# Optimization experiments

Hardware: AMD Instinct MI355X
Metric: run time of the kernel (lower is better)

The kernel has to match this reference:

```python
import jax, jax.numpy as jnp
import numpy as np

PC_RANGE = [-51.2, -51.2, -5.0, 51.2, 51.2, 3.0]
VOXEL = [0.1, 0.1, 0.2]
OSF = 8
NUM_PRIOR = 100
C = 256
BN_EPS = 1e-5
LN_EPS = 1e-5


def _conv(x, w, pad):
    # x: [B,C,H,W], w: [O,I,kh,kw]
    return jax.lax.conv_general_dilated(
        x, w, window_strides=(1, 1), padding=[(pad, pad), (pad, pad)],
        dimension_numbers=('NCHW', 'OIHW', 'NCHW'))


def _bn(x, g, b, m, v):
    scale = (g / jnp.sqrt(v + BN_EPS))[None, :, None, None]
    return (x - m[None, :, None, None]) * scale + b[None, :, None, None]


def setup_inputs() -> dict:
    key = jax.random.key(0)
    ks = jax.random.split(key, 24)
    s3 = 1.0 / np.sqrt(C * 9)
    s1 = 1.0 / np.sqrt(C)
    inp = {
        'bev_feat': jax.random.normal(ks[0], (4, C, 128, 128), jnp.float32),
        'template_anchor': jax.random.normal(ks[1], (4, 900, 11), jnp.float32),
        # shared_conv: 3x3 conv (no bias) + BN(eval) + ReLU
        'shared_w': jax.random.normal(ks[2], (C, C, 3, 3), jnp.float32) * s3,
        'bn1_g': jax.random.normal(ks[3], (C,), jnp.float32) * 0.1 + 1.0,
        'bn1_b': jax.random.normal(ks[4], (C,), jnp.float32) * 0.1,
        'bn1_m': jax.random.normal(ks[5], (C,), jnp.float32) * 0.1,
        'bn1_v': jax.random.uniform(ks[6], (C,), jnp.float32) + 0.5,
        # objectness: 3x3 conv (no bias) + BN + ReLU + 1x1 conv (bias=-2)
        'obj_w1': jax.random.normal(ks[7], (C, C, 3, 3), jnp.float32) * s3,
        'bn2_g': jax.random.normal(ks[8], (C,), jnp.float32) * 0.1 + 1.0,
        'bn2_b': jax.random.normal(ks[9], (C,), jnp.float32) * 0.1,
        'bn2_m': jax.random.normal(ks[10], (C,), jnp.float32) * 0.1,
        'bn2_v': jax.random.uniform(ks[11], (C,), jnp.float32) + 0.5,
        'obj_w2': jax.random.normal(ks[12], (1, C, 1, 1), jnp.float32) * s1,
        'obj_b2': jnp.full((1,), -2.0, jnp.float32),
        # feat_proj: Linear + LN + ReLU + Linear
        'fp_w1': jax.random.normal(ks[13], (C, C), jnp.float32) * s1,
        'fp_b1': jax.random.normal(ks[14], (C,), jnp.float32) * 0.01,
        'ln_g': jnp.ones((C,), jnp.float32),
        'ln_b': jnp.zeros((C,), jnp.float32),
        'fp_w2': jax.random.normal(ks[15], (C, C), jnp.float32) * s1,
        'fp_b2': jax.random.normal(ks[16], (C,), jnp.float32) * 0.01,
        # geometry heads (1x1 convs, bias init 0)
        'z_w': jax.random.normal(ks[17], (1, C, 1, 1), jnp.float32) * s1,
        'z_b': jnp.zeros((1,), jnp.float32),
        'dim_w': jax.random.normal(ks[18], (3, C, 1, 1), jnp.float32) * s1,
        'dim_b': jnp.zeros((3,), jnp.float32),
        'yaw_w': jax.random.normal(ks[19], (2, C, 1, 1), jnp.float32) * s1,
        'yaw_b': jnp.zeros((2,), jnp.float32),
        'vel_w': jax.random.normal(ks[20], (2, C, 1, 1), jnp.float32) * s1,
        'vel_b': jnp.zeros((2,), jnp.float32),
    }
    return inp


def _forward(bev_feat, template_anchor, shared_w, bn1_g, bn1_b, bn1_m, bn1_v,
             obj_w1, bn2_g, bn2_b, bn2_m, bn2_v, obj_w2, obj_b2,
             fp_w1, fp_b1, ln_g, ln_b, fp_w2, fp_b2,
             z_w, z_b, dim_w, dim_b, yaw_w, yaw_b, vel_w, vel_b):
    B, Cc, H, W = bev_feat.shape
    # shared_conv
    feat = jax.nn.relu(_bn(_conv(bev_feat, shared_w, 1), bn1_g, bn1_b, bn1_m, bn1_v))
    # objectness heatmap
    h = jax.nn.relu(_bn(_conv(feat, obj_w1, 1), bn2_g, bn2_b, bn2_m, bn2_v))
    heatmap = jax.nn.sigmoid(_conv(h, obj_w2, 0) + obj_b2[None, :, None, None])
    score = heatmap.reshape(B, H * W)
    K = min(NUM_PRIOR, H * W, template_anchor.shape[1])
    topk_score, topk_inds = jax.lax.top_k(score, K)  # [B,K]
    ys = topk_inds // W
    xs = topk_inds % W
    # gather BEV features at topk locations: [B,K,C]
    feat_flat = feat.reshape(B, Cc, H * W).transpose(0, 2, 1)
    gathered = jnp.take_along_axis(feat_flat, topk_inds[:, :, None], axis=1)
    # feat_proj: Linear + LN + ReLU + Linear
    x = gathered @ fp_w1.T + fp_b1
    mu = jnp.mean(x, axis=-1, keepdims=True)
    var = jnp.mean((x - mu) ** 2, axis=-1, keepdims=True)
    x = (x - mu) / jnp.sqrt(var + LN_EPS) * ln_g + ln_b
    x = jax.nn.relu(x)
    prior_feature = x @ fp_w2.T + fp_b2
    prior_feature = prior_feature * (1.0 + topk_score[:, :, None])
    # geometry heads (1x1 convs == linear on gathered features)
    z_pred = gathered @ z_w[:, :, 0, 0].T + z_b      # [B,K,1]
    dim_pred = gathered @ dim_w[:, :, 0, 0].T + dim_b  # [B,K,3]
    yaw_pred = gathered @ yaw_w[:, :, 0, 0].T + yaw_b  # [B,K,2]
    vel_pred = gathered @ vel_w[:, :, 0, 0].T + vel_b  # [B,K,2]
    # anchor update
    pa = template_anchor[:, :K, :]
    x_metric = (xs.astype(pa.dtype) + 0.5) * (VOXEL[0] * OSF) + PC_RANGE[0]
    y_metric = (ys.astype(pa.dtype) + 0.5) * (VOXEL[1] * OSF) + PC_RANGE[1]
    z_new = pa[..., 2] + 0.5 * z_pred[..., 0]
    dims_new = pa[..., 3:6] + 0.2 * jnp.clip(dim_pred, -1.0, 1.0)
    yaw = jnp.tanh(yaw_pred)
    nrm = jnp.maximum(jnp.sqrt(jnp.sum(yaw * yaw, axis=-1, keepdims=True)), 1e-6)
    yaw_new = 0.7 * pa[..., 6:8] + 0.3 * (yaw / nrm)
    vel_new = pa[..., 8:10] + 0.2 * jnp.clip(vel_pred, -2.0, 2.0)
    prior_anchor = jnp.concatenate([
        x_metric[..., None], y_metric[..., None], z_new[..., None],
        dims_new, yaw_new, vel_new, pa[..., 10:]], axis=-1)
    return prior_feature, prior_anchor, topk_score


def reference(bev_feat, template_anchor, shared_w, bn1_g, bn1_b, bn1_m, bn1_v,
              obj_w1, bn2_g, bn2_b, bn2_m, bn2_v, obj_w2, obj_b2,
              fp_w1, fp_b1, ln_g, ln_b, fp_w2, fp_b2,
              z_w, z_b, dim_w, dim_b, yaw_w, yaw_b, vel_w, vel_b):
    return _forward(bev_feat, template_anchor, shared_w, bn1_g, bn1_b, bn1_m, bn1_v,
                    obj_w1, bn2_g, bn2_b, bn2_m, bn2_v, obj_w2, obj_b2,
                    fp_w1, fp_b1, ln_g, ln_b, fp_w2, fp_b2,
                    z_w, z_b, dim_w, dim_b, yaw_w, yaw_b, vel_w, vel_b)
```

## Files before the change

kernel.cpp:

```cpp
#include <hip/hip_runtime.h>
#include <math.h>


typedef __attribute__((ext_vector_type(8))) short bf16x8;
typedef __attribute__((ext_vector_type(4))) float f32x4;

#define HW 16384
#define WPITCH 130
#define CCAP 192
#define PSTR 28
#define WSO_XN    0ULL
#define WSO_FEATB 34078720ULL
#define WSO_WP1   68157440ULL
#define WSO_WP2   69337088ULL
#define WSO_BNP   70516736ULL
#define WSO_LOG   70521856ULL
#define WSO_CAND  70784000ULL
#define WSO_CNT   70787072ULL
#define WSO_EXL   70787136ULL
#define WSO_TIDX  70790208ULL
#define WSO_TLOG  70791808ULL
#define WSO_W1N   70793408ULL
#define WSO_W2N   73152704ULL
#define WSO_A1P   WSO_XN
#define WSO_ACC2  28311552ULL

__device__ __forceinline__ float bf2f(short s) {
  return __uint_as_float(((unsigned)(unsigned short)s) << 16);
}
__device__ __forceinline__ short f2bf(float f) {
  unsigned u = __float_as_uint(f);
  u += 0x7fffu + ((u >> 16) & 1u);
  return (short)(u >> 16);
}
__device__ __forceinline__ void gll16(const void* g, void* l) {
  __builtin_amdgcn_global_load_lds(
      (const __attribute__((address_space(1))) void*)g,
      (__attribute__((address_space(3))) void*)l, 16, 0, 0);
}

__global__ void wprep2(const float* __restrict__ s1, const float* __restrict__ s2,
                       short* __restrict__ wp1, short* __restrict__ wp2,
                       float* __restrict__ wn1, float* __restrict__ wn2) {
  int bx = blockIdx.x;
  const float* src;
  short* wp;
  float* wn;
  if (bx >= 2304) {
    src = s2; wp = wp2; wn = wn2; bx -= 2304;
  } else {
    src = s1; wp = wp1; wn = wn1;
  }
  int i = bx * 256 + threadIdx.x;
  float v = src[i];
  int k = i % 9;
  int r = i / 9;
  int ci = r & 255;
  int co = r >> 8;
  wp[(k * 256 + co) * 256 + ci] = f2bf(v);
  wn[(ci * 9 + k) * 256 + co] = v;
}

__global__ void smallprep(const float* g1, const float* b1, const float* m1,
                          const float* v1, const float* g2, const float* b2,
                          const float* m2, const float* v2, const float* w2,
                          const float* ob2, float* __restrict__ bnp,
                          short* __restrict__ xn, short* __restrict__ featb,
                          float* __restrict__ logits) {
  const int blk = blockIdx.x, t = threadIdx.x;
  if (blk < 1024) {
    int i = blk * 256 + t;
    int c = i & 255;
    int r = i >> 8;
    int nh = r >> 1;
    int side = r & 1;
    size_t off = ((size_t)nh * WPITCH + (side ? 129 : 0)) * 256 + c;
    xn[off] = 0;
    featb[off] = 0;
  } else if (blk < 1280) {
    logits[(blk - 1024) * 256 + t] = ob2[0];
  } else {
    float s1 = g1[t] / sqrtf(v1[t] + 1e-5f);
    bnp[t] = s1;
    bnp[256 + t] = b1[t] - m1[t] * s1;
    float s2 = g2[t] / sqrtf(v2[t] + 1e-5f);
    bnp[512 + t] = s2;
    bnp[768 + t] = b2[t] - m2[t] * s2;
    bnp[1024 + t] = w2[t];
  }
}

__global__ __launch_bounds__(256) void nchw2nhwc(const float* __restrict__ in,
                                                 short* __restrict__ out) {
  __shared__ short tl[64 * 66];
  int n = blockIdx.z, c0 = blockIdx.y * 64, s0 = blockIdx.x * 64;
  int sl = threadIdx.x & 63, cl = threadIdx.x >> 6;
  for (int p = 0; p < 16; ++p) {
    int c = cl + p * 4;
    tl[c * 66 + sl] = f2bf(in[(((size_t)(n * 256 + c0 + c)) << 14) + s0 + sl]);
  }
  __syncthreads();
  int co = threadIdx.x & 63, so = threadIdx.x >> 6;
  for (int p = 0; p < 16; ++p) {
    int S = s0 + so + p * 4;
    int h = S >> 7, w = S & 127;
    out[(((size_t)(n * 128 + h)) * WPITCH + w + 1) * 256 + c0 + co] =
        tl[co * 66 + (so + p * 4)];
  }
}

template <int OUT_LOGITS>
__global__ __launch_bounds__(256) void conv3x3(const short* __restrict__ inp,
                                               const short* __restrict__ wp,
                                               const float* __restrict__ scale,
                                               const float* __restrict__ shift,
                                               const float* __restrict__ w2f,
                                               short* __restrict__ outb,
                                               float* __restrict__ logits) {
  __shared__ short a_sm[132 * 32];
  __shared__ short b_sm[3][128 * 32];
  const int t = threadIdx.x;
  const int wv = t >> 6, lane = t & 63;
  const int l15 = lane & 15, quad = lane >> 4;
  const int tile = blockIdx.x;
  const int img = tile >> 7;
  const int h = tile & 127;
  const int nblk = blockIdx.y;
  const int m0 = (wv & 1) << 6;
  const int n0 = (wv >> 1) << 6;

  f32x4 acc[4][4];
#pragma unroll
  for (int i = 0; i < 4; ++i)
#pragma unroll
    for (int j = 0; j < 4; ++j) {
      acc[i][j][0] = 0.f; acc[i][j][1] = 0.f;
      acc[i][j][2] = 0.f; acc[i][j][3] = 0.f;
    }

  for (int dhi = 0; dhi < 3; ++dhi) {
    const int hy = h + dhi - 1;
    if (hy < 0 || hy > 127) continue;
    const size_t arow = ((size_t)(img * 128 + hy)) * WPITCH;
    const short* wbase = wp + ((size_t)(dhi * 3 * 256 + nblk * 128)) * 256;

    for (int c0 = 0; c0 < 256; c0 += 32) {
      __syncthreads();
#pragma unroll
      for (int j = 0; j < 2; ++j) {
        const int seg = (j << 6) + (t >> 2);
        const int cc = t & 3;
        gll16(inp + (arow + seg) * 256 + c0 + cc * 8,
              a_sm + ((size_t)((j << 8) + t)) * 8);
      }
      if (t < 32) {
        const int r = t >> 4, dw = t & 15;
        const int* gsrc = (const int*)(inp + (arow + 128 + r) * 256 + c0) + dw;
        ((int*)a_sm)[(128 + r) * 16 + dw] = *gsrc;
      }
#pragma unroll
      for (int dwi = 0; dwi < 3; ++dwi) {
        const short* wtap = wbase + (size_t)dwi * 65536;
#pragma unroll
        for (int j = 0; j < 2; ++j) {
          const int nrow = (j << 6) + (t >> 2);
          const int cc = t & 3;
          gll16(wtap + (size_t)nrow * 256 + c0 + cc * 8,
                b_sm[dwi] + ((size_t)((j << 8) + t)) * 8);
        }
      }
      __syncthreads();

#pragma unroll
      for (int dwi = 0; dwi < 3; ++dwi) {
        bf16x8 af[4], bfr[4];
#pragma unroll
        for (int i = 0; i < 4; ++i)
          af[i] = *(const bf16x8*)(a_sm + (dwi + m0 + i * 16 + l15) * 32 + quad * 8);
#pragma unroll
        for (int i = 0; i < 4; ++i)
          bfr[i] = *(const bf16x8*)(b_sm[dwi] + (n0 + i * 16 + l15) * 32 + quad * 8);
#pragma unroll
        for (int i = 0; i < 4; ++i)
#pragma unroll
          for (int j = 0; j < 4; ++j)
            acc[i][j] = __builtin_amdgcn_mfma_f32_16x16x32_bf16(af[i], bfr[j],
                                                                acc[i][j], 0, 0, 0);
      }
    }
  }

  float sc[4], sh[4], wf[4];
#pragma unroll
  for (int j = 0; j < 4; ++j) {
    const int co = nblk * 128 + n0 + j * 16 + l15;
    sc[j] = scale[co];
    sh[j] = shift[co];
    if (OUT_LOGITS) wf[j] = w2f[co];
  }
  if (OUT_LOGITS) {
    float* lrow = logits + ((size_t)img << 14) + (h << 7);
#pragma unroll
    for (int i = 0; i < 4; ++i) {
#pragma unroll
      for (int r = 0; r < 4; ++r) {
        float part = 0.f;
#pragma unroll
        for (int j = 0; j < 4; ++j) {
          float v = fmaxf(acc[i][j][r] * sc[j] + sh[j], 0.f);
          part += v * wf[j];
        }
        part += __shfl_xor(part, 1);
        part += __shfl_xor(part, 2);
        part += __shfl_xor(part, 4);
        part += __shfl_xor(part, 8);
        if (l15 == 0)
          atomicAdd(&lrow[m0 + i * 16 + quad * 4 + r], part);
      }
    }
  } else {
    const size_t obase = ((size_t)(img * 128 + h)) * WPITCH + 1;
#pragma unroll
    for (int i = 0; i < 4; ++i) {
#pragma unroll
      for (int j = 0; j < 4; ++j) {
        const int co = nblk * 128 + n0 + j * 16 + l15;
#pragma unroll
        for (int r = 0; r < 4; ++r) {
          const int m = m0 + i * 16 + quad * 4 + r;
          float v = fmaxf(acc[i][j][r] * sc[j] + sh[j], 0.f);
          outb[(obase + m) * 256 + co] = f2bf(v);
        }
      }
    }
  }
}

__global__ __launch_bounds__(1024) void topk_radix(const float* __restrict__ logits,
                                                   int* __restrict__ cand,
                                                   int* __restrict__ cnt_out) {
  __shared__ int hist[2048];
  __shared__ int wsum[16];
  __shared__ unsigned sel_bin;
  __shared__ int sel_above;
  __shared__ int cntr;
  const int b = blockIdx.x, t = threadIdx.x;
  const int lane = t & 63, wid = t >> 6;
  const float* L = logits + (size_t)b * HW;
  const int base = t * 16;
  unsigned kv[16];
#pragma unroll
  for (int i = 0; i < 4; ++i) {
    float4 v = *(const float4*)(L + base + i * 4);
    float f4[4] = {v.x, v.y, v.z, v.w};
#pragma unroll
    for (int j = 0; j < 4; ++j) {
      unsigned u = __float_as_uint(f4[j]);
      kv[i * 4 + j] = u ^ (((unsigned)((int)u >> 31)) | 0x80000000u);
    }
  }
  unsigned prefix = 0, pmask = 0;
  int need = 128;
  const int shifts[3] = {21, 10, 0};
  const int nbs[3] = {2048, 2048, 1024};

  for (int lev = 0; lev < 3; ++lev) {
    const int shift = shifts[lev];
    const int nb = nbs[lev];
    hist[t] = 0;
    hist[t + 1024] = 0;
    __syncthreads();
#pragma unroll
    for (int i = 0; i < 16; ++i)
      if ((kv[i] & pmask) == prefix)
        atomicAdd(&hist[(kv[i] >> shift) & (nb - 1)], 1);
    __syncthreads();
    const int cs = nb >> 10;
    const int bin_hi = nb - 1 - t * cs;
    const int c_hi = hist[bin_hi];
    const int c_lo = (cs == 2) ? hist[bin_hi - 1] : 0;
    const int s = c_hi + c_lo;
    int inc = s;
    for (int off = 1; off < 64; off <<= 1) {
      int nbr = __shfl_up(inc, off);
      if (lane >= off) inc += nbr;
    }
    if (lane == 63) wsum[wid] = inc;
    __syncthreads();
    if (wid == 0) {
      int wv = (lane < 16) ? wsum[lane] : 0;
      for (int off = 1; off < 16; off <<= 1) {
        int nbr = __shfl_up(wv, off);
        if (lane >= off) wv += nbr;
      }
      if (lane < 16) wsum[lane] = wv;
    }
    __syncthreads();
    const int excl = inc - s + (wid ? wsum[wid - 1] : 0);
    if (excl < need && need <= excl + s) {
      if (need <= excl + c_hi) {
        sel_bin = (unsigned)bin_hi;
        sel_above = excl;
      } else {
        sel_bin = (unsigned)(bin_hi - 1);
        sel_above = excl + c_hi;
      }
    }
    __syncthreads();
    prefix |= sel_bin << shift;
    pmask |= ((unsigned)(nb - 1)) << shift;
    need -= sel_above;
    __syncthreads();
  }
  if (t == 0) cntr = 0;
  __syncthreads();
#pragma unroll
  for (int i = 0; i < 16; ++i) {
    if (kv[i] >= prefix) {
      int p = atomicAdd(&cntr, 1);
      if (p < CCAP) cand[b * CCAP + p] = base + i;
    }
  }
  __syncthreads();
  if (t == 0) cnt_out[b] = (cntr < CCAP) ? cntr : CCAP;
}

__device__ __forceinline__ void wload4(const float* __restrict__ wr,
                                       float w[4][9]) {
#pragma unroll
  for (int k = 0; k < 9; ++k)
#pragma unroll
    for (int h = 0; h < 4; ++h)
      w[h][k] = wr[k * 256 + (h << 6)];
}

__device__ __forceinline__ void conv_step(const float* __restrict__ pc,
                                          const float w[4][9], float a[4][9]) {
  float xp[28];
  const float4* pr = (const float4*)pc;
#pragma unroll
  for (int q = 0; q < 7; ++q) {
    float4 v = pr[q];
    xp[q * 4 + 0] = v.x; xp[q * 4 + 1] = v.y;
    xp[q * 4 + 2] = v.z; xp[q * 4 + 3] = v.w;
  }
#pragma unroll
  for (int py = 0; py < 3; ++py)
#pragma unroll
    for (int px = 0; px < 3; ++px)
#pragma unroll
      for (int ky = 0; ky < 3; ++ky)
#pragma unroll
        for (int kx = 0; kx < 3; ++kx) {
          const float xv = xp[(py + ky) * 5 + px + kx];
          const int pp = py * 3 + px, kk = ky * 3 + kx;
          a[0][pp] += w[0][kk] * xv;
          a[1][pp] += w[1][kk] * xv;
          a[2][pp] += w[2][kk] * xv;
          a[3][pp] += w[3][kk] * xv;
        }
}

__global__ __launch_bounds__(256, 2) void rescore_a(
    const float* __restrict__ bev, const float* __restrict__ w1n,
    const int* __restrict__ cand, const int* __restrict__ cnt,
    float* __restrict__ a1part) {
  const int bx = blockIdx.x, b = blockIdx.y, z = blockIdx.z;
  const int t = threadIdx.x;
  const int n = cnt[b];
  const int c0 = bx * 4;
  if (c0 >= n) return;
  const int nc = (n - c0 < 4) ? (n - c0) : 4;
  const int ci0 = z << 6;
  __shared__ float patch[4 * 64 * PSTR];

  {
    const int TE = nc * 1600;
    int sg[4];
#pragma unroll
    for (int g = 0; g < 4; ++g) {
      int cc = c0 + g;
      sg[g] = cand[b * CCAP + ((cc < n) ? cc : (n - 1))];
    }
#pragma unroll
    for (int k = 0; k < 25; ++k) {
      int e = t + (k << 8);
      if (e < TE) {
        int g = (e >= 3200) ? ((e >= 4800) ? 3 : 2) : ((e >= 1600) ? 1 : 0);
        int rem = e - g * 1600;
        int ci = rem / 25;
        int rj = rem - ci * 25;
        int r = rj / 5;
        int j = rj - r * 5;
        int s = sg[g];
        int hy = (s >> 7) - 2 + r, wx = (s & 127) - 2 + j;
        float v = 0.f;
        if (hy >= 0 && hy < 128 && wx >= 0 && wx < 128)
          v = bev[(((size_t)(b * 256 + ci0 + ci)) << 14) + (hy << 7) + wx];
        patch[(g * 64 + ci) * PSTR + rj] = v;
      } else {
        int g2z = (e >= 3200) ? ((e >= 4800) ? 3 : 2) : 1;
        int rem = e - g2z * 1600;
        int ci = rem / 25;
        int rj = rem - ci * 25;
        patch[(g2z * 64 + ci) * PSTR + rj] = 0.f;
      }
    }
  }
  __syncthreads();

  const int col = t & 63;
  const int g = t >> 6;
  float a[4][9];
#pragma unroll
  for (int h = 0; h < 4; ++h)
#pragma unroll
    for (int p = 0; p < 9; ++p) a[h][p] = 0.f;

  const float* pbase = patch + (g << 6) * PSTR;
  const float* wbase = w1n + (size_t)ci0 * 2304 + col;

  float wA[4][9], wB[4][9];
  wload4(wbase, wA);
  for (int ci = 0; ci < 64; ci += 2) {
    wload4(wbase + (size_t)(ci + 1) * 2304, wB);
    conv_step(pbase + ci * PSTR, wA, a);
    if (ci + 2 < 64)
      wload4(wbase + (size_t)(ci + 2) * 2304, wA);
    conv_step(pbase + (ci + 1) * PSTR, wB, a);
  }

  if (g < nc) {
    const int c = c0 + g;
    float* dst =
        a1part + ((((size_t)(b * CCAP + c) * 4 + z) * 9) << 8) + col;
#pragma unroll
    for (int p = 0; p < 9; ++p)
#pragma unroll
      for (int h = 0; h < 4; ++h)
        dst[(p << 8) + (h << 6)] = a[h][p];
  }
}

__global__ __launch_bounds__(256) void rescore_b(const float* __restrict__ a1part,
                                                 const float* __restrict__ w2n,
                                                 const float* __restrict__ bnp,
                                                 const int* __restrict__ cnt,
                                                 float* __restrict__ acc2) {
  const int bx = blockIdx.x, b = blockIdx.y, z = blockIdx.z;
  const int t = threadIdx.x;
  const int n = cnt[b];
  const int cbase = bx * 8;
  if (cbase >= n) return;
  const int zb = z << 6;
  __shared__ float f9[8 * 64 * 12];

  const int cf = t & 63;
  const int pg = t >> 6;
  const int cfg = zb + cf;
  const float sc1 = bnp[cfg], sh1 = bnp[256 + cfg];
#pragma unroll
  for (int g = 0; g < 8; ++g) {
    const int c = cbase + g;
    if (c < n) {
      const float* src =
          a1part + ((((size_t)(b * CCAP + c)) * 36) << 8) + cfg;
      for (int p = pg; p < 9; p += 4) {
        float v = src[(size_t)(0 * 9 + p) << 8] + src[(size_t)(1 * 9 + p) << 8] +
                  src[(size_t)(2 * 9 + p) << 8] + src[(size_t)(3 * 9 + p) << 8];
        f9[(g * 64 + cf) * 12 + p] = fmaxf(v * sc1 + sh1, 0.f);
      }
    } else {
      for (int p = pg; p < 9; p += 4) f9[(g * 64 + cf) * 12 + p] = 0.f;
    }
  }
  __syncthreads();

  float acc[8];
#pragma unroll
  for (int g = 0; g < 8; ++g) acc[g] = 0.f;
  for (int ci = 0; ci < 64; ++ci) {
    const float* wr = w2n + (size_t)(zb + ci) * 2304 + t;
    float w9[9];
#pragma unroll
    for (int k = 0; k < 9; ++k) w9[k] = wr[k * 256];
#pragma unroll
    for (int g = 0; g < 8; ++g) {
      const float4* fp = (const float4*)(f9 + (g * 64 + ci) * 12);
      float4 f0 = fp[0], f1 = fp[1], f2 = fp[2];
      acc[g] += w9[0] * f0.x;
      acc[g] += w9[1] * f0.y;
      acc[g] += w9[2] * f0.z;
      acc[g] += w9[3] * f0.w;
      acc[g] += w9[4] * f1.x;
      acc[g] += w9[5] * f1.y;
      acc[g] += w9[6] * f1.z;
      acc[g] += w9[7] * f1.w;
      acc[g] += w9[8] * f2.x;
    }
  }
#pragma unroll
  for (int g = 0; g < 8; ++g) {
    const int c = cbase + g;
    if (c < n)
      acc2[((((size_t)(b * CCAP + c)) * 4 + z) << 8) + t] = acc[g];
  }
}

__global__ __launch_bounds__(256) void rescore_c(const float* __restrict__ acc2,
                                                 const float* __restrict__ bnp,
                                                 const float* __restrict__ b2,
                                                 const int* __restrict__ cnt,
                                                 float* __restrict__ exlog) {
  const int bx = blockIdx.x, b = blockIdx.y, t = threadIdx.x;
  const int lane = t & 63, wid = t >> 6;
  const int n = cnt[b];
  const int c = bx * 4 + wid;
  if (c >= n) return;
  const float* src = acc2 + (((size_t)(b * CCAP + c)) << 10);
  float p = 0.f;
#pragma unroll
  for (int j = 0; j < 4; ++j) {
    const int co = lane + j * 64;
    float v = ((src[co] + src[256 + co]) + src[512 + co]) + src[768 + co];
    p += fmaxf(v * bnp[512 + co] + bnp[768 + co], 0.f) * bnp[1024 + co];
  }
  for (int off = 32; off; off >>= 1) p += __shfl_xor(p, off);
  if (lane == 0) exlog[b * CCAP + c] = p + b2[0];
}

__global__ __launch_bounds__(CCAP) void final_topk(const float* __restrict__ exlog,
                                                   const int* __restrict__ cand,
                                                   const int* __restrict__ cnt,
                                                   int* __restrict__ tidx,
                                                   float* __restrict__ tlog) {
  const int b = blockIdx.x, t = threadIdx.x;
  __shared__ float v[CCAP];
  __shared__ int si[CCAP];
  const int n = cnt[b];
  float mv = (t < n) ? exlog[b * CCAP + t] : -3.0e38f;
  int s = (t < n) ? cand[b * CCAP + t] : 0x7FFFFFFF;
  v[t] = mv;
  si[t] = s;
  __syncthreads();
  int rank = 0;
  for (int j = 0; j < CCAP; ++j) {
    float vj = v[j];
    int sj = si[j];
    if (vj > mv || (vj == mv && sj < s)) ++rank;
  }
  if (t < n && rank < 100) {
    tidx[b * 100 + rank] = s;
    tlog[b * 100 + rank] = mv;
  }
}

__global__ __launch_bounds__(256) void head_kern(
    const short* __restrict__ featb, const int* __restrict__ tidx,
    const float* __restrict__ tlog, const float* __restrict__ tmpl,
    const float* __restrict__ w1, const float* __restrict__ b1,
    const float* __restrict__ lng, const float* __restrict__ lnb,
    const float* __restrict__ w2, const float* __restrict__ b2,
    const float* __restrict__ zw, const float* __restrict__ zb,
    const float* __restrict__ dmw, const float* __restrict__ dmb,
    const float* __restrict__ yw, const float* __restrict__ yb,
    const float* __restrict__ vw, const float* __restrict__ vb,
    float* __restrict__ out) {
  const int blk = blockIdx.x;
  const int b = blk / 100, q = blk % 100;
  const int t = threadIdx.x;
  const int lane = t & 63, wid = t >> 6;
  __shared__ float g[256];
  __shared__ float sx[256];
  __shared__ float red[4];
  __shared__ float heads[8];

  const int s = tidx[b * 100 + q];
  const float score = 1.f / (1.f + expf(-tlog[b * 100 + q]));
  const int ys = s >> 7, xs = s & 127;

  g[t] = bf2f(featb[(((size_t)(b * 128 + ys)) * WPITCH + xs + 1) * 256 + t]);
  __syncthreads();

  float x = b1[t];
  {
    const float* wr = w1 + (size_t)t * 256;
    for (int i = 0; i < 256; i += 4) {
      float4 wv = *(const float4*)(wr + i);
      x += g[i] * wv.x + g[i + 1] * wv.y + g[i + 2] * wv.z + g[i + 3] * wv.w;
    }
  }
  float sum = x;
  for (int off = 32; off; off >>= 1) sum += __shfl_xor(sum, off);
  if (lane == 0) red[wid] = sum;
  __syncthreads();
  float mu = (red[0] + red[1] + red[2] + red[3]) * (1.f / 256.f);
  __syncthreads();
  float d = x - mu;
  float q2 = d * d;
  for (int off = 32; off; off >>= 1) q2 += __shfl_xor(q2, off);
  if (lane == 0) red[wid] = q2;
  __syncthreads();
  float var = (red[0] + red[1] + red[2] + red[3]) * (1.f / 256.f);
  float xn = d * (1.f / sqrtf(var + 1e-5f)) * lng[t] + lnb[t];
  xn = fmaxf(xn, 0.f);
  sx[t] = xn;
  __syncthreads();
  float pf = b2[t];
  {
    const float* wr = w2 + (size_t)t * 256;
    for (int i = 0; i < 256; i += 4) {
      float4 wv = *(const float4*)(wr + i);
      pf += sx[i] * wv.x + sx[i + 1] * wv.y + sx[i + 2] * wv.z + sx[i + 3] * wv.w;
    }
  }
  pf *= (1.f + score);
  out[(size_t)(b * 100 + q) * 256 + t] = pf;

  const int k = t >> 5, l = t & 31;
  const float* hw;
  float hb;
  if (k == 0)      { hw = zw;                 hb = zb[0]; }
  else if (k < 4)  { hw = dmw + (k - 1) * 256; hb = dmb[k - 1]; }
  else if (k < 6)  { hw = yw + (k - 4) * 256;  hb = yb[k - 4]; }
  else             { hw = vw + (k - 6) * 256;  hb = vb[k - 6]; }
  float hp = 0.f;
#pragma unroll
  for (int r = 0; r < 8; ++r) {
    int i = l + r * 32;
    hp += g[i] * hw[i];
  }
  for (int off = 16; off; off >>= 1) hp += __shfl_xor(hp, off);
  if (l == 0) heads[k] = hp + hb;
  __syncthreads();

  if (t == 0) {
    const float* pa = tmpl + ((size_t)b * 900 + q) * 11;
    float p[11];
#pragma unroll
    for (int i = 0; i < 11; ++i) p[i] = pa[i];
    float a[11];
    a[0] = ((float)xs + 0.5f) * 0.8f - 51.2f;
    a[1] = ((float)ys + 0.5f) * 0.8f - 51.2f;
    a[2] = p[2] + 0.5f * heads[0];
#pragma unroll
    for (int i = 0; i < 3; ++i)
      a[3 + i] = p[3 + i] + 0.2f * fminf(fmaxf(heads[1 + i], -1.f), 1.f);
    float t0 = tanhf(heads[4]), t1 = tanhf(heads[5]);
    float nrm = fmaxf(sqrtf(t0 * t0 + t1 * t1), 1e-6f);
    a[6] = 0.7f * p[6] + 0.3f * t0 / nrm;
    a[7] = 0.7f * p[7] + 0.3f * t1 / nrm;
    a[8] = p[8] + 0.2f * fminf(fmaxf(heads[6], -2.f), 2.f);
    a[9] = p[9] + 0.2f * fminf(fmaxf(heads[7], -2.f), 2.f);
    a[10] = p[10];
    float* oa = out + 102400 + (size_t)(b * 100 + q) * 11;
#pragma unroll
    for (int i = 0; i < 11; ++i) oa[i] = a[i];
    out[106800 + b * 100 + q] = score;
  }
}

extern "C" void kernel_launch(void* const* d_in, const int* in_sizes, int n_in,
                              void* d_out, int out_size, void* d_ws, size_t ws_size,
                              hipStream_t stream) {
  (void)in_sizes; (void)n_in; (void)out_size; (void)ws_size;
  char* ws = (char*)d_ws;
  short* xn     = (short*)(ws + WSO_XN);
  short* featb  = (short*)(ws + WSO_FEATB);
  short* wp1    = (short*)(ws + WSO_WP1);
  short* wp2    = (short*)(ws + WSO_WP2);
  float* bnp    = (float*)(ws + WSO_BNP);
  float* logits = (float*)(ws + WSO_LOG);
  int*   cand   = (int*)(ws + WSO_CAND);
  int*   cnt    = (int*)(ws + WSO_CNT);
  float* exl    = (float*)(ws + WSO_EXL);
  int*   tidx   = (int*)(ws + WSO_TIDX);
  float* tlog   = (float*)(ws + WSO_TLOG);
  float* w1n    = (float*)(ws + WSO_W1N);
  float* w2n    = (float*)(ws + WSO_W2N);
  float* a1p    = (float*)(ws + WSO_A1P);
  float* acc2   = (float*)(ws + WSO_ACC2);

  const float* bev = (const float*)d_in[0];

  wprep2<<<4608, 256, 0, stream>>>((const float*)d_in[2], (const float*)d_in[7],
                                   wp1, wp2, w1n, w2n);
  smallprep<<<1281, 256, 0, stream>>>(
      (const float*)d_in[3], (const float*)d_in[4], (const float*)d_in[5],
      (const float*)d_in[6], (const float*)d_in[8], (const float*)d_in[9],
      (const float*)d_in[10], (const float*)d_in[11], (const float*)d_in[12],
      (const float*)d_in[13], bnp, xn, featb, logits);
  nchw2nhwc<<<dim3(256, 4, 4), 256, 0, stream>>>(bev, xn);
  conv3x3<0><<<dim3(512, 2), 256, 0, stream>>>(xn, wp1, bnp, bnp + 256,
                                               nullptr, featb, nullptr);
  conv3x3<1><<<dim3(512, 2), 256, 0, stream>>>(featb, wp2, bnp + 512, bnp + 768,
                                               bnp + 1024, nullptr, logits);
  topk_radix<<<4, 1024, 0, stream>>>(logits, cand, cnt);
  rescore_a<<<dim3(CCAP / 4, 4, 4), 256, 0, stream>>>(bev, w1n, cand, cnt, a1p);
  rescore_b<<<dim3(CCAP / 8, 4, 4), 256, 0, stream>>>(a1p, w2n, bnp, cnt, acc2);
  rescore_c<<<dim3(CCAP / 4, 4), 256, 0, stream>>>(acc2, bnp,
                                                   (const float*)d_in[13], cnt,
                                                   exl);
  final_topk<<<4, CCAP, 0, stream>>>(exl, cand, cnt, tidx, tlog);
  head_kern<<<400, 256, 0, stream>>>(
      featb, tidx, tlog, (const float*)d_in[1],
      (const float*)d_in[14], (const float*)d_in[15], (const float*)d_in[16],
      (const float*)d_in[17], (const float*)d_in[18], (const float*)d_in[19],
      (const float*)d_in[20], (const float*)d_in[21], (const float*)d_in[22],
      (const float*)d_in[23], (const float*)d_in[24], (const float*)d_in[25],
      (const float*)d_in[26], (const float*)d_in[27], (float*)d_out);
}
```

Before: 540.3 us.

## Remap rescore_a threads to share weights across two candidates per block

Each rescore_a block now covers 2 candidates with 128 threads instead of 4 candidates with 256 threads. Each thread computes 2 output channels for both candidates, so every weight load is reused for two patches instead of one. Blocks become smaller and twice as numerous, and each block skips its second candidate when it falls beyond the count. This cuts redundant global weight loads per candidate. In exchange, per-thread register use and grid size both go up.

```diff
diff --git a/kernel.cpp b/kernel.cpp
--- a/kernel.cpp
+++ b/kernel.cpp
@@ -325,17 +325,17 @@
   if (t == 0) cnt_out[b] = (cntr < CCAP) ? cntr : CCAP;
 }
 
-__device__ __forceinline__ void wload4(const float* __restrict__ wr,
-                                       float w[4][9]) {
-#pragma unroll
-  for (int k = 0; k < 9; ++k)
-#pragma unroll
-    for (int h = 0; h < 4; ++h)
-      w[h][k] = wr[k * 256 + (h << 6)];
-}
-
-__device__ __forceinline__ void conv_step(const float* __restrict__ pc,
-                                          const float w[4][9], float a[4][9]) {
+__device__ __forceinline__ void wload2(const float* __restrict__ wr,
+                                       float w[2][9]) {
+#pragma unroll
+  for (int k = 0; k < 9; ++k) {
+    w[0][k] = wr[k * 256];
+    w[1][k] = wr[k * 256 + 128];
+  }
+}
+
+__device__ __forceinline__ void conv_step2(const float* __restrict__ pc,
+                                           const float w[2][9], float a[2][9]) {
   float xp[28];
   const float4* pr = (const float4*)pc;
 #pragma unroll
@@ -356,37 +356,35 @@
           const int pp = py * 3 + px, kk = ky * 3 + kx;
           a[0][pp] += w[0][kk] * xv;
           a[1][pp] += w[1][kk] * xv;
-          a[2][pp] += w[2][kk] * xv;
-          a[3][pp] += w[3][kk] * xv;
         }
 }
 
-__global__ __launch_bounds__(256, 2) void rescore_a(
+__global__ __launch_bounds__(128, 2) void rescore_a(
     const float* __restrict__ bev, const float* __restrict__ w1n,
     const int* __restrict__ cand, const int* __restrict__ cnt,
     float* __restrict__ a1part) {
   const int bx = blockIdx.x, b = blockIdx.y, z = blockIdx.z;
   const int t = threadIdx.x;
   const int n = cnt[b];
-  const int c0 = bx * 4;
+  const int c0 = bx * 2;
   if (c0 >= n) return;
-  const int nc = (n - c0 < 4) ? (n - c0) : 4;
+  const int nc = (n - c0 < 2) ? (n - c0) : 2;
   const int ci0 = z << 6;
-  __shared__ float patch[4 * 64 * PSTR];
+  __shared__ float patch[2 * 64 * PSTR];
 
   {
     const int TE = nc * 1600;
-    int sg[4];
-#pragma unroll
-    for (int g = 0; g < 4; ++g) {
+    int sg[2];
+#pragma unroll
+    for (int g = 0; g < 2; ++g) {
       int cc = c0 + g;
       sg[g] = cand[b * CCAP + ((cc < n) ? cc : (n - 1))];
     }
 #pragma unroll
     for (int k = 0; k < 25; ++k) {
-      int e = t + (k << 8);
+      int e = t + (k << 7);
       if (e < TE) {
-        int g = (e >= 3200) ? ((e >= 4800) ? 3 : 2) : ((e >= 1600) ? 1 : 0);
+        int g = (e >= 1600) ? 1 : 0;
         int rem = e - g * 1600;
         int ci = rem / 25;
         int rj = rem - ci * 25;
@@ -399,46 +397,51 @@
           v = bev[(((size_t)(b * 256 + ci0 + ci)) << 14) + (hy << 7) + wx];
         patch[(g * 64 + ci) * PSTR + rj] = v;
       } else {
-        int g2z = (e >= 3200) ? ((e >= 4800) ? 3 : 2) : 1;
-        int rem = e - g2z * 1600;
+        int rem = e - 1600;
         int ci = rem / 25;
         int rj = rem - ci * 25;
-        patch[(g2z * 64 + ci) * PSTR + rj] = 0.f;
-      }
-    }
-  }
-  __syncthreads();
-
-  const int col = t & 63;
-  const int g = t >> 6;
-  float a[4][9];
-#pragma unroll
-  for (int h = 0; h < 4; ++h)
-#pragma unroll
-    for (int p = 0; p < 9; ++p) a[h][p] = 0.f;
-
-  const float* pbase = patch + (g << 6) * PSTR;
+        patch[(64 + ci) * PSTR + rj] = 0.f;
+      }
+    }
+  }
+  __syncthreads();
+
+  const int col = t;
+  float aA[2][9], aB[2][9];
+#pragma unroll
+  for (int h = 0; h < 2; ++h)
+#pragma unroll
+    for (int p = 0; p < 9; ++p) { aA[h][p] = 0.f; aB[h][p] = 0.f; }
+
+  const float* p0 = patch;
+  const float* p1 = patch + 64 * PSTR;
   const float* wbase = w1n + (size_t)ci0 * 2304 + col;
 
-  float wA[4][9], wB[4][9];
-  wload4(wbase, wA);
+  float wA[2][9], wB[2][9];
+  wload2(wbase, wA);
   for (int ci = 0; ci < 64; ci += 2) {
-    wload4(wbase + (size_t)(ci + 1) * 2304, wB);
-    conv_step(pbase + ci * PSTR, wA, a);
+    wload2(wbase + (size_t)(ci + 1) * 2304, wB);
+    conv_step2(p0 + ci * PSTR, wA, aA);
+    conv_step2(p1 + ci * PSTR, wA, aB);
     if (ci + 2 < 64)
-      wload4(wbase + (size_t)(ci + 2) * 2304, wA);
-    conv_step(pbase + (ci + 1) * PSTR, wB, a);
-  }
-
-  if (g < nc) {
+      wload2(wbase + (size_t)(ci + 2) * 2304, wA);
+    conv_step2(p0 + (ci + 1) * PSTR, wB, aA);
+    conv_step2(p1 + (ci + 1) * PSTR, wB, aB);
+  }
+
+#pragma unroll
+  for (int g = 0; g < 2; ++g) {
     const int c = c0 + g;
-    float* dst =
-        a1part + ((((size_t)(b * CCAP + c) * 4 + z) * 9) << 8) + col;
-#pragma unroll
-    for (int p = 0; p < 9; ++p)
-#pragma unroll
-      for (int h = 0; h < 4; ++h)
-        dst[(p << 8) + (h << 6)] = a[h][p];
+    if (c < n) {
+      const float (*a)[9] = g ? aB : aA;
+      float* dst =
+          a1part + ((((size_t)(b * CCAP + c) * 4 + z) * 9) << 8) + col;
+#pragma unroll
+      for (int p = 0; p < 9; ++p) {
+        dst[p << 8] = a[0][p];
+        dst[(p << 8) + 128] = a[1][p];
+      }
+    }
   }
 }
 
@@ -696,7 +699,7 @@
   conv3x3<1><<<dim3(512, 2), 256, 0, stream>>>(featb, wp2, bnp + 512, bnp + 768,
                                                bnp + 1024, nullptr, logits);
   topk_radix<<<4, 1024, 0, stream>>>(logits, cand, cnt);
-  rescore_a<<<dim3(CCAP / 4, 4, 4), 256, 0, stream>>>(bev, w1n, cand, cnt, a1p);
+  rescore_a<<<dim3(CCAP / 2, 4, 4), 128, 0, stream>>>(bev, w1n, cand, cnt, a1p);
   rescore_b<<<dim3(CCAP / 8, 4, 4), 256, 0, stream>>>(a1p, w2n, bnp, cnt, acc2);
   rescore_c<<<dim3(CCAP / 4, 4), 256, 0, stream>>>(acc2, bnp,
                                                    (const float*)d_in[13], cnt,
```

New measurement: 573.5 us. +6.1%, slower.

## Compute two output rows per conv block to reuse weight tiles

Applied to the files above, without the earlier changes.

Each conv3x3 block now computes two adjacent output rows instead of one. The three weight-tap tiles loaded into LDS are shared across both rows, which halves weight traffic per output and halves the grid size. The cost is a second accumulator set (128 more fp32 values per thread), which raises register pressure. Launch bounds now ask for two blocks per CU, so spills are possible and occupancy drops to 512 blocks per conv.

```diff
diff --git a/kernel.cpp b/kernel.cpp
--- a/kernel.cpp
+++ b/kernel.cpp
@@ -110,53 +110,75 @@
 }
 
 template <int OUT_LOGITS>
-__global__ __launch_bounds__(256) void conv3x3(const short* __restrict__ inp,
-                                               const short* __restrict__ wp,
-                                               const float* __restrict__ scale,
-                                               const float* __restrict__ shift,
-                                               const float* __restrict__ w2f,
-                                               short* __restrict__ outb,
-                                               float* __restrict__ logits) {
-  __shared__ short a_sm[132 * 32];
+__global__ __launch_bounds__(256, 2) void conv3x3(const short* __restrict__ inp,
+                                                  const short* __restrict__ wp,
+                                                  const float* __restrict__ scale,
+                                                  const float* __restrict__ shift,
+                                                  const float* __restrict__ w2f,
+                                                  short* __restrict__ outb,
+                                                  float* __restrict__ logits) {
+  __shared__ short a_sm[2][132 * 32];
   __shared__ short b_sm[3][128 * 32];
   const int t = threadIdx.x;
   const int wv = t >> 6, lane = t & 63;
   const int l15 = lane & 15, quad = lane >> 4;
   const int tile = blockIdx.x;
-  const int img = tile >> 7;
-  const int h = tile & 127;
+  const int img = tile >> 6;
+  const int h0 = (tile & 63) << 1;
   const int nblk = blockIdx.y;
   const int m0 = (wv & 1) << 6;
   const int n0 = (wv >> 1) << 6;
 
-  f32x4 acc[4][4];
-#pragma unroll
-  for (int i = 0; i < 4; ++i)
-#pragma unroll
-    for (int j = 0; j < 4; ++j) {
-      acc[i][j][0] = 0.f; acc[i][j][1] = 0.f;
-      acc[i][j][2] = 0.f; acc[i][j][3] = 0.f;
-    }
+  f32x4 acc[2][4][4];
+#pragma unroll
+  for (int r = 0; r < 2; ++r)
+#pragma unroll
+    for (int i = 0; i < 4; ++i)
+#pragma unroll
+      for (int j = 0; j < 4; ++j) {
+        acc[r][i][j][0] = 0.f; acc[r][i][j][1] = 0.f;
+        acc[r][i][j][2] = 0.f; acc[r][i][j][3] = 0.f;
+      }
 
   for (int dhi = 0; dhi < 3; ++dhi) {
-    const int hy = h + dhi - 1;
-    if (hy < 0 || hy > 127) continue;
-    const size_t arow = ((size_t)(img * 128 + hy)) * WPITCH;
+    const int hy0 = h0 + dhi - 1;
+    const int hy1 = hy0 + 1;
+    const bool v0 = (hy0 >= 0) && (hy0 <= 127);
+    const bool v1 = (hy1 <= 127);
+    const size_t arow0 = ((size_t)(img * 128 + hy0)) * WPITCH;
+    const size_t arow1 = ((size_t)(img * 128 + hy1)) * WPITCH;
     const short* wbase = wp + ((size_t)(dhi * 3 * 256 + nblk * 128)) * 256;
 
     for (int c0 = 0; c0 < 256; c0 += 32) {
       __syncthreads();
-#pragma unroll
-      for (int j = 0; j < 2; ++j) {
-        const int seg = (j << 6) + (t >> 2);
-        const int cc = t & 3;
-        gll16(inp + (arow + seg) * 256 + c0 + cc * 8,
-              a_sm + ((size_t)((j << 8) + t)) * 8);
-      }
-      if (t < 32) {
-        const int r = t >> 4, dw = t & 15;
-        const int* gsrc = (const int*)(inp + (arow + 128 + r) * 256 + c0) + dw;
-        ((int*)a_sm)[(128 + r) * 16 + dw] = *gsrc;
+      if (v0) {
+#pragma unroll
+        for (int j = 0; j < 2; ++j) {
+          const int seg = (j << 6) + (t >> 2);
+          const int cc = t & 3;
+          gll16(inp + (arow0 + seg) * 256 + c0 + cc * 8,
+                a_sm[0] + ((size_t)((j << 8) + t)) * 8);
+        }
+      }
+      if (v1) {
+#pragma unroll
+        for (int j = 0; j < 2; ++j) {
+          const int seg = (j << 6) + (t >> 2);
+          const int cc = t & 3;
+          gll16(inp + (arow1 + seg) * 256 + c0 + cc * 8,
+                a_sm[1] + ((size_t)((j << 8) + t)) * 8);
+        }
+      }
+      if (t < 64) {
+        const int row = t >> 5;
+        const bool vr = row ? v1 : v0;
+        if (vr) {
+          const size_t ar = row ? arow1 : arow0;
+          const int rem = t & 31;
+          const int r2 = rem >> 4, dw = rem & 15;
+          const int* gsrc = (const int*)(inp + (ar + 128 + r2) * 256 + c0) + dw;
+          ((int*)a_sm[row])[(128 + r2) * 16 + dw] = *gsrc;
+        }
       }
 #pragma unroll
       for (int dwi = 0; dwi < 3; ++dwi) {
@@ -173,19 +195,34 @@
 
 #pragma unroll
       for (int dwi = 0; dwi < 3; ++dwi) {
-        bf16x8 af[4], bfr[4];
-#pragma unroll
-        for (int i = 0; i < 4; ++i)
-          af[i] = *(const bf16x8*)(a_sm + (dwi + m0 + i * 16 + l15) * 32 + quad * 8);
+        bf16x8 bfr[4];
 #pragma unroll
         for (int i = 0; i < 4; ++i)
           bfr[i] = *(const bf16x8*)(b_sm[dwi] + (n0 + i * 16 + l15) * 32 + quad * 8);
-#pragma unroll
-        for (int i = 0; i < 4; ++i)
-#pragma unroll
-          for (int j = 0; j < 4; ++j)
-            acc[i][j] = __builtin_amdgcn_mfma_f32_16x16x32_bf16(af[i], bfr[j],
-                                                                acc[i][j], 0, 0, 0);
+        if (v0) {
+          bf16x8 af[4];
+#pragma unroll
+          for (int i = 0; i < 4; ++i)
+            af[i] = *(const bf16x8*)(a_sm[0] + (dwi + m0 + i * 16 + l15) * 32 + quad * 8);
+#pragma unroll
+          for (int i = 0; i < 4; ++i)
+#pragma unroll
+            for (int j = 0; j < 4; ++j)
+              acc[0][i][j] = __builtin_amdgcn_mfma_f32_16x16x32_bf16(
+                  af[i], bfr[j], acc[0][i][j], 0, 0, 0);
+        }
+        if (v1) {
+          bf16x8 af[4];
+#pragma unroll
+          for (int i = 0; i < 4; ++i)
+            af[i] = *(const bf16x8*)(a_sm[1] + (dwi + m0 + i * 16 + l15) * 32 + quad * 8);
+#pragma unroll
+          for (int i = 0; i < 4; ++i)
+#pragma unroll
+            for (int j = 0; j < 4; ++j)
+              acc[1][i][j] = __builtin_amdgcn_mfma_f32_16x16x32_bf16(
+                  af[i], bfr[j], acc[1][i][j], 0, 0, 0);
+        }
       }
     }
   }
@@ -198,38 +235,41 @@
     sh[j] = shift[co];
     if (OUT_LOGITS) wf[j] = w2f[co];
   }
-  if (OUT_LOGITS) {
-    float* lrow = logits + ((size_t)img << 14) + (h << 7);
-#pragma unroll
-    for (int i = 0; i < 4; ++i) {
-#pragma unroll
-      for (int r = 0; r < 4; ++r) {
-        float part = 0.f;
+#pragma unroll
+  for (int r = 0; r < 2; ++r) {
+    if (OUT_LOGITS) {
+      float* lrow = logits + ((size_t)img << 14) + ((h0 + r) << 7);
+#pragma unroll
+      for (int i = 0; i < 4; ++i) {
+#pragma unroll
+        for (int rg = 0; rg < 4; ++rg) {
+          float part = 0.f;
+#pragma unroll
+          for (int j = 0; j < 4; ++j) {
+            float v = fmaxf(acc[r][i][j][rg] * sc[j] + sh[j], 0.f);
+            part += v * wf[j];
+          }
+          part += __shfl_xor(part, 1);
+          part += __shfl_xor(part, 2);
+          part += __shfl_xor(part, 4);
+          part += __shfl_xor(part, 8);
+          if (l15 == 0)
+            atomicAdd(&lrow[m0 + i * 16 + quad * 4 + rg], part);
+        }
+      }
+    } else {
+      const size_t obase = ((size_t)(img * 128 + h0 + r)) * WPITCH + 1;
+#pragma unroll
+      for (int i = 0; i < 4; ++i) {
 #pragma unroll
         for (int j = 0; j < 4; ++j) {
-          float v = fmaxf(acc[i][j][r] * sc[j] + sh[j], 0.f);
-          part += v * wf[j];
-        }
-        part += __shfl_xor(part, 1);
-        part += __shfl_xor(part, 2);
-        part += __shfl_xor(part, 4);
-        part += __shfl_xor(part, 8);
-        if (l15 == 0)
-          atomicAdd(&lrow[m0 + i * 16 + quad * 4 + r], part);
-      }
-    }
-  } else {
-    const size_t obase = ((size_t)(img * 128 + h)) * WPITCH + 1;
-#pragma unroll
-    for (int i = 0; i < 4; ++i) {
-#pragma unroll
-      for (int j = 0; j < 4; ++j) {
-        const int co = nblk * 128 + n0 + j * 16 + l15;
-#pragma unroll
-        for (int r = 0; r < 4; ++r) {
-          const int m = m0 + i * 16 + quad * 4 + r;
-          float v = fmaxf(acc[i][j][r] * sc[j] + sh[j], 0.f);
-          outb[(obase + m) * 256 + co] = f2bf(v);
+          const int co = nblk * 128 + n0 + j * 16 + l15;
+#pragma unroll
+          for (int rg = 0; rg < 4; ++rg) {
+            const int m = m0 + i * 16 + quad * 4 + rg;
+            float v = fmaxf(acc[r][i][j][rg] * sc[j] + sh[j], 0.f);
+            outb[(obase + m) * 256 + co] = f2bf(v);
+          }
         }
       }
     }
@@ -691,9 +731,9 @@
       (const float*)d_in[10], (const float*)d_in[11], (const float*)d_in[12],
       (const float*)d_in[13], bnp, xn, featb, logits);
   nchw2nhwc<<<dim3(256, 4, 4), 256, 0, stream>>>(bev, xn);
-  conv3x3<0><<<dim3(512, 2), 256, 0, stream>>>(xn, wp1, bnp, bnp + 256,
+  conv3x3<0><<<dim3(256, 2), 256, 0, stream>>>(xn, wp1, bnp, bnp + 256,
                                                nullptr, featb, nullptr);
-  conv3x3<1><<<dim3(512, 2), 256, 0, stream>>>(featb, wp2, bnp + 512, bnp + 768,
+  conv3x3<1><<<dim3(256, 2), 256, 0, stream>>>(featb, wp2, bnp + 512, bnp + 768,
                                                bnp + 1024, nullptr, logits);
   topk_radix<<<4, 1024, 0, stream>>>(logits, cand, cnt);
   rescore_a<<<dim3(CCAP / 4, 4, 4), 256, 0, stream>>>(bev, w1n, cand, cnt, a1p);
```

Result: faster. 494.7 us (-8.4%).
